# Kernel tuning notes

Hardware: AMD Instinct MI355X
Metric: run time of the kernel (lower is better)

## Reference

```python
import jax, jax.numpy as jnp
import numpy as np

XBOUND = (-51.2, 51.2, 0.8)
YBOUND = (-51.2, 51.2, 0.8)
ZBOUND = (-10.0, 10.0, 20.0)
DBOUND = (1.0, 60.0, 1.0)
IMG_H, IMG_W = 256, 704
DOWNSAMPLE = 16
CAM_C = 64
OUT_C = 64
D = int((DBOUND[1] - DBOUND[0]) / DBOUND[2])      # 59
NX = int((XBOUND[1] - XBOUND[0]) / XBOUND[2])     # 128
NY = int((YBOUND[1] - YBOUND[0]) / YBOUND[2])     # 128
NZ = int((ZBOUND[1] - ZBOUND[0]) / ZBOUND[2])     # 1
FH, FW = IMG_H // DOWNSAMPLE, IMG_W // DOWNSAMPLE # 16, 44
DX = jnp.array([XBOUND[2], YBOUND[2], ZBOUND[2]], dtype=jnp.float32)
BX = jnp.array([XBOUND[0] + XBOUND[2] / 2.0, YBOUND[0] + YBOUND[2] / 2.0, ZBOUND[0] + ZBOUND[2] / 2.0], dtype=jnp.float32)


def make_frustum():
    ds = jnp.arange(DBOUND[0], DBOUND[1], DBOUND[2], dtype=jnp.float32)   # [D]
    xs = jnp.linspace(0.0, IMG_W - 1.0, FW, dtype=jnp.float32)            # [FW]
    ys = jnp.linspace(0.0, IMG_H - 1.0, FH, dtype=jnp.float32)            # [FH]
    d = jnp.broadcast_to(ds[:, None, None], (D, FH, FW))
    x = jnp.broadcast_to(xs[None, None, :], (D, FH, FW))
    y = jnp.broadcast_to(ys[None, :, None], (D, FH, FW))
    return jnp.stack([x, y, d], axis=-1)                                  # [D,FH,FW,3]


def get_geometry(rots, trans, intrins, post_rots, post_trans):
    # rots/intrins/post_rots: [B,N,3,3]; trans/post_trans: [B,N,3]
    frustum = make_frustum()                                              # [D,FH,FW,3]
    pts = frustum[None, None] - post_trans[:, :, None, None, None]        # [B,N,D,FH,FW,3]
    pts = jnp.einsum('bnij,bndhwj->bndhwi', jnp.linalg.inv(post_rots), pts)
    pts = jnp.concatenate([pts[..., :2] * pts[..., 2:3], pts[..., 2:3]], axis=-1)
    comb = jnp.matmul(rots, jnp.linalg.inv(intrins))
    pts = jnp.einsum('bnij,bndhwj->bndhwi', comb, pts)
    return pts + trans[:, :, None, None, None]


def forward(x, rots, trans, intrins, post_rots, post_trans, w_depth, b_depth):
    B, N, C_in, H, W = x.shape
    # 1x1 conv == channel matmul
    y = jnp.einsum('bnchw,oc->bnohw', x, w_depth) + b_depth[None, None, :, None, None]
    depth = jax.nn.softmax(y[:, :, :D], axis=2)              # [B,N,D,H,W]
    context = y[:, :, D:]                                    # [B,N,OUT_C,H,W]
    outer = depth[:, :, :, None] * context[:, :, None, :]    # [B,N,D,OUT_C,H,W]
    outer = jnp.transpose(outer, (0, 1, 2, 4, 5, 3))         # [B,N,D,H,W,OUT_C]

    geom = jax.lax.stop_gradient(get_geometry(rots, trans, intrins, post_rots, post_trans))
    # torch .long() truncates toward zero -> jnp.trunc
    g = jnp.trunc((geom.reshape(-1, 3) - (BX - DX / 2.0)) / DX).astype(jnp.int32)  # [P,3]
    kept = ((g[:, 0] >= 0) & (g[:, 0] < NX) &
            (g[:, 1] >= 0) & (g[:, 1] < NY) &
            (g[:, 2] >= 0) & (g[:, 2] < NZ))
    batch_ix = jnp.repeat(jnp.arange(B, dtype=jnp.int32), N * D * H * W)
    ranks = batch_ix * (NX * NY * NZ) + g[:, 0] + g[:, 1] * NX + g[:, 2] * NX * NY
    # segment-sum over voxel ranks == sort+cumsum trick + scatter in the original
    feats = jnp.where(kept[:, None], outer.reshape(-1, OUT_C), 0.0)
    ranks = jnp.where(kept, ranks, 0)
    bev = jax.ops.segment_sum(feats, ranks, num_segments=B * NZ * NY * NX)
    bev = bev.reshape(B, NZ, NY, NX, OUT_C).transpose(0, 4, 1, 2, 3).sum(axis=2)
    return bev  # [B, OUT_C, NY, NX]


def setup_inputs() -> dict:
    key = jax.random.key(0)
    B, N = 4, 6
    ks = jax.random.split(key, 8)
    cam2ego = jnp.array([[0.0, 0.0, 1.0], [-1.0, 0.0, 0.0], [0.0, -1.0, 0.0]], dtype=jnp.float32)
    rots = jnp.broadcast_to(cam2ego, (B, N, 3, 3)) + 0.02 * jax.random.normal(ks[0], (B, N, 3, 3), dtype=jnp.float32)
    trans = 1.0 * jax.random.normal(ks[1], (B, N, 3), dtype=jnp.float32)
    K = jnp.array([[700.0, 0.0, IMG_W / 2.0], [0.0, 700.0, IMG_H / 2.0], [0.0, 0.0, 1.0]], dtype=jnp.float32)
    intrins = jnp.broadcast_to(K, (B, N, 3, 3)) + 0.1 * jax.random.normal(ks[2], (B, N, 3, 3), dtype=jnp.float32)
    post_rots = jnp.broadcast_to(jnp.eye(3, dtype=jnp.float32), (B, N, 3, 3)) + 0.01 * jax.random.normal(ks[3], (B, N, 3, 3), dtype=jnp.float32)
    post_trans = 0.1 * jax.random.normal(ks[4], (B, N, 3), dtype=jnp.float32)
    x = jax.random.normal(ks[5], (B, N, CAM_C, FH, FW), dtype=jnp.float32)
    w_depth = 0.05 * jax.random.normal(ks[6], (D + OUT_C, CAM_C), dtype=jnp.float32)
    b_depth = jnp.zeros((D + OUT_C,), dtype=jnp.float32)
    return {"x": x, "rots": rots, "trans": trans, "intrins": intrins,
            "post_rots": post_rots, "post_trans": post_trans,
            "w_depth": w_depth, "b_depth": b_depth}


def reference(x, rots, trans, intrins, post_rots, post_trans, w_depth, b_depth):
    return forward(x, rots, trans, intrins, post_rots, post_trans, w_depth, b_depth)
```

## Files before the change

kernel.cpp:

```cpp
#include <hip/hip_runtime.h>
#include <math.h>

#define Bc 4
#define Nc 6
#define Dc 59
#define FHc 16
#define FWc 44
#define Cc 64
#define OCc 123
#define NXc 128
#define NYc 128
#define NVOX (Bc*NXc*NYc)
#define NBLK (Bc*Nc*FWc)

#define WS_ACC 0
#define WS_CAM ((size_t)16777216)
#define WS_WDT ((size_t)16781312)

template<bool FMA>
__device__ __forceinline__ float mulsub(float a, float b, float c) {
    if (FMA) return __fmaf_rn(-a, b, c);
    return __fadd_rn(c, __fmul_rn(-a, b));
}

template<bool FMA>
__device__ __forceinline__ void lu_inv3x3T(const float* __restrict__ m, float* __restrict__ o) {
    float A[3][3] = {{m[0],m[3],m[6]},{m[1],m[4],m[7]},{m[2],m[5],m[8]}};
    int piv0, piv1;
    {
        float a0=fabsf(A[0][0]), a1=fabsf(A[1][0]), a2=fabsf(A[2][0]);
        int p = 0; float mx = a0;
        if (a1 > mx) { mx = a1; p = 1; }
        if (a2 > mx) { mx = a2; p = 2; }
        piv0 = p;
        if (p != 0) { for (int k=0;k<3;++k){ float t=A[0][k]; A[0][k]=A[p][k]; A[p][k]=t; } }
        const float d = __fdiv_rn(1.0f, A[0][0]);
        A[1][0] = __fmul_rn(A[1][0], d);
        A[2][0] = __fmul_rn(A[2][0], d);
        #pragma unroll
        for (int i=1;i<3;++i)
            #pragma unroll
            for (int j=1;j<3;++j)
                A[i][j] = mulsub<FMA>(A[i][0], A[0][j], A[i][j]);
    }
    {
        float a1=fabsf(A[1][1]), a2=fabsf(A[2][1]);
        int p = (a2 > a1) ? 2 : 1;
        piv1 = p;
        if (p != 1) { for (int k=0;k<3;++k){ float t=A[1][k]; A[1][k]=A[p][k]; A[p][k]=t; } }
        const float d = __fdiv_rn(1.0f, A[1][1]);
        A[2][1] = __fmul_rn(A[2][1], d);
        A[2][2] = mulsub<FMA>(A[2][1], A[1][2], A[2][2]);
    }
    float B[3][3] = {{1.f,0.f,0.f},{0.f,1.f,0.f},{0.f,0.f,1.f}};
    if (piv0 != 0) { for (int k=0;k<3;++k){ float t=B[0][k]; B[0][k]=B[piv0][k]; B[piv0][k]=t; } }
    if (piv1 != 1) { for (int k=0;k<3;++k){ float t=B[1][k]; B[1][k]=B[piv1][k]; B[piv1][k]=t; } }
    #pragma unroll
    for (int j=0;j<3;++j) {
        B[1][j] = mulsub<FMA>(A[1][0], B[0][j], B[1][j]);
        B[2][j] = mulsub<FMA>(A[2][0], B[0][j], B[2][j]);
        B[2][j] = mulsub<FMA>(A[2][1], B[1][j], B[2][j]);
        B[2][j] = __fdiv_rn(B[2][j], A[2][2]);
        B[0][j] = mulsub<FMA>(A[0][2], B[2][j], B[0][j]);
        B[1][j] = mulsub<FMA>(A[1][2], B[2][j], B[1][j]);
        B[1][j] = __fdiv_rn(B[1][j], A[1][1]);
        B[0][j] = mulsub<FMA>(A[0][1], B[1][j], B[0][j]);
        B[0][j] = __fdiv_rn(B[0][j], A[0][0]);
    }
    o[0]=B[0][0]; o[1]=B[1][0]; o[2]=B[2][0];
    o[3]=B[0][1]; o[4]=B[1][1]; o[5]=B[2][1];
    o[6]=B[0][2]; o[7]=B[1][2]; o[8]=B[2][2];
}

template<bool FMA>
__device__ __forceinline__ float dot3(float a0,float a1,float a2,float b0,float b1,float b2){
    if (FMA) return __fmaf_rn(a2,b2, __fmaf_rn(a1,b1, __fmul_rn(a0,b0)));
    return __fadd_rn(__fadd_rn(__fmul_rn(a0,b0), __fmul_rn(a1,b1)), __fmul_rn(a2,b2));
}

__global__ __launch_bounds__(256) void prep(
    const float* __restrict__ wd, const float* __restrict__ rots,
    const float* __restrict__ intrins, const float* __restrict__ post_rots,
    float* __restrict__ wdT2, float* __restrict__ camMat)
{
    const int idx = blockIdx.x*256 + threadIdx.x;
    if (idx < OCc*Cc) {
        const int o = idx >> 6, c = idx & 63;
        const int slot = (o < 64) ? (o << 1) : (((o - 64) << 1) | 1);
        wdT2[(c << 7) + slot] = wd[idx];
    }
    if (idx >= OCc*Cc && idx < OCc*Cc + 320) {
        const int k = idx - OCc*Cc;
        const int c = k / 5, o = 59 + (k % 5);
        wdT2[(c << 7) + (o << 1) + 1] = 0.0f;
    }
    if (blockIdx.x == 0 && threadIdx.x < 48) {
        const int cam = threadIdx.x >> 1;
        const int var = threadIdx.x & 1;
        const float* pr = post_rots + cam*9;
        const float* ro = rots      + cam*9;
        const float* it = intrins   + cam*9;
        float PRi[9], INi[9], CM[9];
        if (var == 0) { lu_inv3x3T<true >(pr, PRi); lu_inv3x3T<true >(it, INi); }
        else          { lu_inv3x3T<false>(pr, PRi); lu_inv3x3T<false>(it, INi); }
        #pragma unroll
        for (int r2 = 0; r2 < 3; ++r2)
            #pragma unroll
            for (int c2 = 0; c2 < 3; ++c2)
                CM[r2*3+c2] = dot3<true>(ro[r2*3+0], ro[r2*3+1], ro[r2*3+2],
                                         INi[0*3+c2], INi[1*3+c2], INi[2*3+c2]);
        float* dst = camMat + (size_t)(cam*2 + var)*18;
        #pragma unroll
        for (int k = 0; k < 9; ++k) { dst[k] = PRi[k]; dst[9+k] = CM[k]; }
    }
}

template<bool FMA>
__device__ __forceinline__ int geom_light(
    const float* __restrict__ PRi, const float* __restrict__ CM,
    float pt0, float pt1, float pt2, float tr0, float tr1, float tr2,
    float u, float v, float dval, int b)
{
    const float p0 = __fsub_rn(u,    pt0);
    const float p1 = __fsub_rn(v,    pt1);
    const float p2 = __fsub_rn(dval, pt2);
    const float q0 = dot3<FMA>(PRi[0],PRi[1],PRi[2], p0,p1,p2);
    const float q1 = dot3<FMA>(PRi[3],PRi[4],PRi[5], p0,p1,p2);
    const float q2 = dot3<FMA>(PRi[6],PRi[7],PRi[8], p0,p1,p2);
    const float r0 = __fmul_rn(q0, q2);
    const float r1 = __fmul_rn(q1, q2);
    const float s0 = __fadd_rn(dot3<FMA>(CM[0],CM[1],CM[2], r0,r1,q2), tr0);
    const float s1 = __fadd_rn(dot3<FMA>(CM[3],CM[4],CM[5], r0,r1,q2), tr1);
    const float s2 = __fadd_rn(dot3<FMA>(CM[6],CM[7],CM[8], r0,r1,q2), tr2);
    const float CX  = -51.200000762939453f;
    const float DXf =  0.80000001192092896f;
    const float gx = __fdiv_rn(__fsub_rn(s0, CX), DXf);
    const float gy = __fdiv_rn(__fsub_rn(s1, CX), DXf);
    const float gz = __fdiv_rn(__fsub_rn(s2, -10.0f), 20.0f);
    const bool kept = (gx > -1.0f) && (gx < 128.0f) &&
                      (gy > -1.0f) && (gy < 128.0f) &&
                      (gz > -1.0f) && (gz < 1.0f);
    return kept ? (b*(NXc*NYc) + ((int)gy)*NXc + (int)gx) : -1;
}

__global__ __launch_bounds__(256, 4) void lss_main(
    const float* __restrict__ x, const float* __restrict__ trans,
    const float* __restrict__ post_trans, const float* __restrict__ bd,
    const float* __restrict__ wdT2, const float* __restrict__ camMat,
    float* __restrict__ acc)
{
    const int blk = blockIdx.x;
    const int wi  = blk % FWc;
    const int cam = blk / FWc;
    const int b   = cam / Nc;
    const int t = threadIdx.x;
    const int wave = t >> 6, lane = t & 63;

    __shared__ float  xsT[64][16];
    __shared__ float  yv[16][60];
    __shared__ float  ctxT[64][18];
    __shared__ float4 geo[Dc][16];

    {
        const float* xb = x + (size_t)cam*64*(FHc*FWc) + wi;
        for (int idx = t; idx < 1024; idx += 256) {
            const int c = idx >> 4, hi = idx & 15;
            xsT[c][hi] = xb[(size_t)c*(FHc*FWc) + hi*FWc];
        }
    }
    __syncthreads();

    {
        const int hi0 = wave << 2;
        float a0[4] = {0.f,0.f,0.f,0.f}, a1[4] = {0.f,0.f,0.f,0.f};
        const float2* wrow = (const float2*)wdT2 + lane;
        #pragma unroll 8
        for (int c = 0; c < 64; ++c) {
            const float2 wv = wrow[c << 6];
            const float4 xv = *(const float4*)&xsT[c][hi0];
            a0[0] = __fmaf_rn(wv.x, xv.x, a0[0]); a1[0] = __fmaf_rn(wv.y, xv.x, a1[0]);
            a0[1] = __fmaf_rn(wv.x, xv.y, a0[1]); a1[1] = __fmaf_rn(wv.y, xv.y, a1[1]);
            a0[2] = __fmaf_rn(wv.x, xv.z, a0[2]); a1[2] = __fmaf_rn(wv.y, xv.z, a1[2]);
            a0[3] = __fmaf_rn(wv.x, xv.w, a0[3]); a1[3] = __fmaf_rn(wv.y, xv.w, a1[3]);
        }
        const float b0 = bd[lane];
        const float b1 = (lane < 59) ? bd[64 + lane] : 0.0f;
        #pragma unroll
        for (int k = 0; k < 4; ++k) {
            const int hi = hi0 + k;
            const float y0 = __fadd_rn(a0[k], b0);
            if (lane < 59) {
                yv[hi][lane] = y0;
                ctxT[lane + 5][hi] = __fadd_rn(a1[k], b1);
            } else {
                ctxT[lane - 59][hi] = y0;
            }
        }
    }
    for (int k = 0; k < 4; ++k) {
        const int hi = (wave << 2) | k;
        float v = (lane < Dc) ? yv[hi][lane] : -INFINITY;
        float m = v;
        #pragma unroll
        for (int off = 32; off; off >>= 1) m = fmaxf(m, __shfl_xor(m, off));
        float e = (lane < Dc) ? expf(__fsub_rn(v, m)) : 0.0f;
        float s = e;
        #pragma unroll
        for (int off = 32; off; off >>= 1) s = __fadd_rn(s, __shfl_xor(s, off));
        if (lane < Dc) yv[hi][lane] = __fdiv_rn(e, s);
    }
    __syncthreads();

    {
        const float pt0 = post_trans[cam*3+0], pt1 = post_trans[cam*3+1], pt2 = post_trans[cam*3+2];
        const float tr0 = trans[cam*3+0],      tr1 = trans[cam*3+1],      tr2 = trans[cam*3+2];
        const float* M0 = camMat + (size_t)(cam*2 + 0)*18;
        const float* M1 = camMat + (size_t)(cam*2 + 1)*18;
        const float u = (float)(wi * (703.0 / 43.0));
        for (int idx = t; idx < 16*Dc; idx += 256) {
            const int d = idx >> 4, hi = idx & 15;
            const float v    = (float)(hi * 17.0);
            const float dval = (float)(1 + d);
            const int vA = geom_light<true >(M0, M0+9, pt0,pt1,pt2, tr0,tr1,tr2, u, v, dval, b);
            const int vB = geom_light<false>(M1, M1+9, pt0,pt1,pt2, tr0,tr1,tr2, u, v, dval, b);
            geo[d][hi] = make_float4(yv[hi][d], __int_as_float(vA), __int_as_float(vB), 0.0f);
        }
    }
    __syncthreads();

    {
        float cx[16];
        #pragma unroll
        for (int h = 0; h < 16; h += 2) {
            const float2 c2 = *(const float2*)&ctxT[lane][h];
            cx[h] = c2.x; cx[h+1] = c2.y;
        }
        for (int d = wave; d < Dc; d += 4) {
            int runVox = -1;
            float accv = 0.0f;
            #pragma unroll
            for (int hi = 0; hi < 16; ++hi) {
                const float4 g = geo[d][hi];
                const float dw = g.x;
                const int vA = __float_as_int(g.y);
                const int vB = __float_as_int(g.z);
                const float cxv = cx[hi];
                if (vA == vB) {
                    if (vA >= 0) {
                        if (vA != runVox) {
                            if (runVox >= 0) atomicAdd(&acc[((size_t)runVox << 6) + lane], accv);
                            runVox = vA; accv = 0.0f;
                        }
                        accv = __fadd_rn(accv, __fmul_rn(dw, cxv));
                    }
                } else {
                    const float hw = __fmul_rn(dw, 0.5f);
                    if (vA >= 0) {
                        if (vA != runVox) {
                            if (runVox >= 0) atomicAdd(&acc[((size_t)runVox << 6) + lane], accv);
                            runVox = vA; accv = 0.0f;
                        }
                        accv = __fadd_rn(accv, __fmul_rn(hw, cxv));
                    }
                    if (vB >= 0) atomicAdd(&acc[((size_t)vB << 6) + lane], __fmul_rn(hw, cxv));
                }
            }
            if (runVox >= 0) atomicAdd(&acc[((size_t)runVox << 6) + lane], accv);
        }
    }
}

__global__ __launch_bounds__(256) void lss_transpose(
    const float* __restrict__ acc, float* __restrict__ out)
{
    __shared__ float tile[64][65];
    const int blk = blockIdx.x;
    const int b = blk >> 8;
    const int pixbase = (blk & 255) * 64;
    const float* src = acc + ((size_t)b*16384 + pixbase)*64;
    const int t = threadIdx.x;
    #pragma unroll
    for (int i = 0; i < 16; ++i) {
        const int e = i*256 + t;
        tile[e & 63][e >> 6] = src[e];
    }
    __syncthreads();
    float* dst = out + (size_t)b*64*16384 + pixbase;
    #pragma unroll
    for (int i = 0; i < 16; ++i) {
        const int e = i*256 + t;
        const int c = e >> 6, p = e & 63;
        dst[(size_t)c*16384 + p] = tile[c][p];
    }
}

extern "C" void kernel_launch(void* const* d_in, const int* in_sizes, int n_in,
                              void* d_out, int out_size, void* d_ws, size_t ws_size,
                              hipStream_t stream) {
    const float* x          = (const float*)d_in[0];
    const float* rots       = (const float*)d_in[1];
    const float* trans      = (const float*)d_in[2];
    const float* intrins    = (const float*)d_in[3];
    const float* post_rots  = (const float*)d_in[4];
    const float* post_trans = (const float*)d_in[5];
    const float* wd         = (const float*)d_in[6];
    const float* bd         = (const float*)d_in[7];
    float* out = (float*)d_out;
    char* ws = (char*)d_ws;

    float* acc    = (float*)(ws + WS_ACC);
    float* camMat = (float*)(ws + WS_CAM);
    float* wdT2   = (float*)(ws + WS_WDT);

    hipMemsetAsync(acc, 0, (size_t)NVOX*64*sizeof(float), stream);
    prep<<<dim3(32), dim3(256), 0, stream>>>(wd, rots, intrins, post_rots, wdT2, camMat);
    lss_main<<<dim3(NBLK), dim3(256), 0, stream>>>(
        x, trans, post_trans, bd, wdT2, camMat, acc);
    lss_transpose<<<dim3(Bc*256), dim3(256), 0, stream>>>(acc, out);
}
```

Baseline: 203.6 us.

## Split depth range across two blocks, fuse accumulator zeroing, vectorize transpose

The main kernel now launches two blocks per pixel column, each handling half the depth bins, so there are twice as many blocks and more are resident per CU. The cost is that each block redundantly recomputes the input load, 1x1 conv and softmax. The separate memset is folded into the prep kernel, which now runs 2048 blocks writing float4 zeros. The transpose kernel switches to float4 global loads and stores. Together these target poor occupancy and launch count in the scatter stage and narrow memory accesses in the transpose.

```diff
diff --git a/kernel.cpp b/kernel.cpp
--- a/kernel.cpp
+++ b/kernel.cpp
@@ -12,6 +12,7 @@
 #define NYc 128
 #define NVOX (Bc*NXc*NYc)
 #define NBLK (Bc*Nc*FWc)
+#define NBLK2 (NBLK*2)
 
 #define WS_ACC 0
 #define WS_CAM ((size_t)16777216)
@@ -81,22 +82,25 @@
 __global__ __launch_bounds__(256) void prep(
     const float* __restrict__ wd, const float* __restrict__ rots,
     const float* __restrict__ intrins, const float* __restrict__ post_rots,
-    float* __restrict__ wdT2, float* __restrict__ camMat)
+    float* __restrict__ wdT2, float* __restrict__ camMat, float4* __restrict__ acc4)
 {
-    const int idx = blockIdx.x*256 + threadIdx.x;
-    if (idx < OCc*Cc) {
-        const int o = idx >> 6, c = idx & 63;
+    const int gid = blockIdx.x*256 + threadIdx.x;
+    const float4 z = make_float4(0.f, 0.f, 0.f, 0.f);
+    acc4[gid] = z;
+    acc4[gid + 524288] = z;
+
+    if (gid < OCc*Cc) {
+        const int o = gid >> 6, c = gid & 63;
         const int slot = (o < 64) ? (o << 1) : (((o - 64) << 1) | 1);
-        wdT2[(c << 7) + slot] = wd[idx];
-    }
-    if (idx >= OCc*Cc && idx < OCc*Cc + 320) {
-        const int k = idx - OCc*Cc;
+        wdT2[(c << 7) + slot] = wd[gid];
+    } else if (gid < OCc*Cc + 320) {
+        const int k = gid - OCc*Cc;
         const int c = k / 5, o = 59 + (k % 5);
         wdT2[(c << 7) + (o << 1) + 1] = 0.0f;
     }
-    if (blockIdx.x == 0 && threadIdx.x < 48) {
-        const int cam = threadIdx.x >> 1;
-        const int var = threadIdx.x & 1;
+    if (gid < 48) {
+        const int cam = gid >> 1;
+        const int var = gid & 1;
         const float* pr = post_rots + cam*9;
         const float* ro = rots      + cam*9;
         const float* it = intrins   + cam*9;
@@ -143,15 +147,19 @@
     return kept ? (b*(NXc*NYc) + ((int)gy)*NXc + (int)gx) : -1;
 }
 
-__global__ __launch_bounds__(256, 4) void lss_main(
+__global__ __launch_bounds__(256, 8) void lss_main(
     const float* __restrict__ x, const float* __restrict__ trans,
     const float* __restrict__ post_trans, const float* __restrict__ bd,
     const float* __restrict__ wdT2, const float* __restrict__ camMat,
     float* __restrict__ acc)
 {
-    const int blk = blockIdx.x;
-    const int wi  = blk % FWc;
-    const int cam = blk / FWc;
+    const int blk2 = blockIdx.x;
+    const int pixblk = blk2 >> 1;
+    const int half = blk2 & 1;
+    const int d0 = half * 30;
+    const int dn = 30 - half;
+    const int wi  = pixblk % FWc;
+    const int cam = pixblk / FWc;
     const int b   = cam / Nc;
     const int t = threadIdx.x;
     const int wave = t >> 6, lane = t & 63;
@@ -159,7 +167,7 @@
     __shared__ float  xsT[64][16];
     __shared__ float  yv[16][60];
     __shared__ float  ctxT[64][18];
-    __shared__ float4 geo[Dc][16];
+    __shared__ float4 geo[30][16];
 
     {
         const float* xb = x + (size_t)cam*64*(FHc*FWc) + wi;
@@ -217,13 +225,14 @@
         const float* M0 = camMat + (size_t)(cam*2 + 0)*18;
         const float* M1 = camMat + (size_t)(cam*2 + 1)*18;
         const float u = (float)(wi * (703.0 / 43.0));
-        for (int idx = t; idx < 16*Dc; idx += 256) {
-            const int d = idx >> 4, hi = idx & 15;
+        for (int idx = t; idx < 16*dn; idx += 256) {
+            const int dd = idx >> 4, hi = idx & 15;
+            const int d = d0 + dd;
             const float v    = (float)(hi * 17.0);
             const float dval = (float)(1 + d);
             const int vA = geom_light<true >(M0, M0+9, pt0,pt1,pt2, tr0,tr1,tr2, u, v, dval, b);
             const int vB = geom_light<false>(M1, M1+9, pt0,pt1,pt2, tr0,tr1,tr2, u, v, dval, b);
-            geo[d][hi] = make_float4(yv[hi][d], __int_as_float(vA), __int_as_float(vB), 0.0f);
+            geo[dd][hi] = make_float4(yv[hi][d], __int_as_float(vA), __int_as_float(vB), 0.0f);
         }
     }
     __syncthreads();
@@ -235,12 +244,12 @@
             const float2 c2 = *(const float2*)&ctxT[lane][h];
             cx[h] = c2.x; cx[h+1] = c2.y;
         }
-        for (int d = wave; d < Dc; d += 4) {
+        for (int dd = wave; dd < dn; dd += 4) {
             int runVox = -1;
             float accv = 0.0f;
             #pragma unroll
             for (int hi = 0; hi < 16; ++hi) {
-                const float4 g = geo[d][hi];
+                const float4 g = geo[dd][hi];
                 const float dw = g.x;
                 const int vA = __float_as_int(g.y);
                 const int vB = __float_as_int(g.z);
@@ -277,20 +286,24 @@
     const int blk = blockIdx.x;
     const int b = blk >> 8;
     const int pixbase = (blk & 255) * 64;
-    const float* src = acc + ((size_t)b*16384 + pixbase)*64;
+    const float4* src4 = (const float4*)(acc + ((size_t)b*16384 + pixbase)*64);
     const int t = threadIdx.x;
     #pragma unroll
-    for (int i = 0; i < 16; ++i) {
-        const int e = i*256 + t;
-        tile[e & 63][e >> 6] = src[e];
+    for (int i = 0; i < 4; ++i) {
+        const int e4 = i*256 + t;
+        const float4 v = src4[e4];
+        const int e = e4 << 2;
+        const int r = e & 63, c = e >> 6;
+        tile[r+0][c] = v.x; tile[r+1][c] = v.y; tile[r+2][c] = v.z; tile[r+3][c] = v.w;
     }
     __syncthreads();
     float* dst = out + (size_t)b*64*16384 + pixbase;
     #pragma unroll
-    for (int i = 0; i < 16; ++i) {
-        const int e = i*256 + t;
-        const int c = e >> 6, p = e & 63;
-        dst[(size_t)c*16384 + p] = tile[c][p];
+    for (int i = 0; i < 4; ++i) {
+        const int idx = i*256 + t;
+        const int c = idx >> 4, p = (idx & 15) << 2;
+        const float4 v = make_float4(tile[c][p], tile[c][p+1], tile[c][p+2], tile[c][p+3]);
+        *(float4*)&dst[(size_t)c*16384 + p] = v;
     }
 }
 
@@ -312,9 +325,9 @@
     float* camMat = (float*)(ws + WS_CAM);
     float* wdT2   = (float*)(ws + WS_WDT);
 
-    hipMemsetAsync(acc, 0, (size_t)NVOX*64*sizeof(float), stream);
-    prep<<<dim3(32), dim3(256), 0, stream>>>(wd, rots, intrins, post_rots, wdT2, camMat);
-    lss_main<<<dim3(NBLK), dim3(256), 0, stream>>>(
+    prep<<<dim3(2048), dim3(256), 0, stream>>>(
+        wd, rots, intrins, post_rots, wdT2, camMat, (float4*)acc);
+    lss_main<<<dim3(NBLK2), dim3(256), 0, stream>>>(
         x, trans, post_trans, bd, wdT2, camMat, acc);
     lss_transpose<<<dim3(Bc*256), dim3(256), 0, stream>>>(acc, out);
 }
```

Result: slower. 220.0 us (+8.0%).
